# Kernel optimization log

Measured on AMD Instinct MI355X. Metric: run time of the kernel, lower is better.

Reference implementation:

```python
import jax, jax.numpy as jnp
import numpy as np

N = 100000
E = 1600000
IN_DIM = 128
OUT_DIM = 64


def setup_inputs() -> dict:
    key = jax.random.key(0)
    k_h, k_ei, k_ew, k_W, k_a = jax.random.split(key, 5)
    h = jax.random.normal(k_h, (N, IN_DIM), dtype=jnp.float32)
    edge_index = jax.random.randint(k_ei, (2, E), 0, N, dtype=jnp.int64)
    edge_weight = jax.random.uniform(k_ew, (E,), dtype=jnp.float32)
    # nn.Linear weights (Kaiming-uniform-ish scale)
    W = jax.random.uniform(k_W, (OUT_DIM, IN_DIM), dtype=jnp.float32,
                           minval=-1.0, maxval=1.0) / np.sqrt(IN_DIM)
    a = jax.random.uniform(k_a, (2 * OUT_DIM,), dtype=jnp.float32,
                           minval=-1.0, maxval=1.0) / np.sqrt(2 * OUT_DIM)
    return {"h": h, "edge_index": edge_index, "edge_weight": edge_weight,
            "W": W, "a": a}


def reference(h, edge_index, edge_weight, W, a):
    # Faithful translation of _GATConvSparse.forward (inference; dropout = identity).
    n = h.shape[0]
    src, dst = edge_index[0], edge_index[1]
    Wh = h @ W.T                                  # (N, out_dim)
    d = Wh.shape[1]
    # a(cat([Wh[src], Wh[dst]])) == Wh[src] @ a[:d] + Wh[dst] @ a[d:]
    alpha = Wh[src] @ a[:d] + Wh[dst] @ a[d:]     # (E,)
    alpha = alpha * edge_weight
    # Buggy-but-faithful 'softmax': segment-sum raw scores onto dst nodes...
    alpha_node = jax.ops.segment_sum(alpha, dst, num_segments=n)   # (N,)
    alpha_exp = jnp.exp(alpha_node - alpha_node.max())             # (N,)
    # ...then normalize per-edge exp(src) by sum of exp(src) over each dst segment.
    denom = jax.ops.segment_sum(alpha_exp[src], dst, num_segments=n)  # (N,)
    alpha_norm = alpha_exp[src] / (denom[dst] + 1e-9)              # (E,)
    out = jax.ops.segment_sum(alpha_norm[:, None] * Wh[src], dst,
                              num_segments=n)                      # (N, out_dim)
    return jax.nn.elu(out)
```

## Files before the change

kernel.cpp:

```cpp
#include <hip/hip_runtime.h>
#include <math.h>

#define Nn 100000
#define Ee 1600000
#define IND 128
#define OUTD 64
#define DPB 64
#define NB 1563
#define CAP 1536
#define GB 1563
#define EB_BLOCKS 391
#define AFIX 1048576.0f

using bf16x8 = __attribute__((ext_vector_type(8))) short;
using f32x4 = __attribute__((ext_vector_type(4))) float;

__device__ __forceinline__ unsigned short f2bf(float f) {
    unsigned u = __float_as_uint(f);
    u = u + 0x7FFFu + ((u >> 16) & 1u);
    return (unsigned short)(u >> 16);
}
__device__ __forceinline__ float bf2f(unsigned short h) {
    return __uint_as_float(((unsigned)h) << 16);
}

__device__ __forceinline__ bool probe64(const void* __restrict__ ei) {
    const long long* p = (const long long*)ei;
    bool ok = true;
#pragma unroll
    for (int i = 0; i < 8; ++i) {
        long long v = p[i];
        ok = ok && (v >= 0 && v < Nn);
    }
    return ok;
}

__device__ __forceinline__ void load_edge(const void* ei, int e, bool is64,
                                          int& s, int& d) {
    if (is64) {
        const long long* p = (const long long*)ei;
        s = (int)p[e];
        d = (int)p[Ee + e];
    } else {
        const int* p = (const int*)ei;
        s = p[e];
        d = p[Ee + e];
    }
}

__device__ __forceinline__ int load_dst(const void* ei, int e, bool is64) {
    if (is64) return (int)((const long long*)ei)[Ee + e];
    return ((const int*)ei)[Ee + e];
}

__global__ __launch_bounds__(256) void k_fused(
    const float* __restrict__ h, const float* __restrict__ W,
    const float* __restrict__ a, unsigned short* __restrict__ Whb,
    float* __restrict__ s1, float* __restrict__ s2,
    const void* __restrict__ ei, int* __restrict__ bcount) {
    __shared__ unsigned short Ash[64][136];
    __shared__ unsigned short Wsh[64][136];
    __shared__ float al[2 * OUTD];
    int bid = blockIdx.x;
    int t = threadIdx.x;

    if (bid < GB) {
        int R = bid * 64;
        for (int i = t; i < 2048; i += 256) {
            float4 v = ((const float4*)W)[i];
            int r = i >> 5, c = (i & 31) << 2;
            unsigned lo = (unsigned)f2bf(v.x) | ((unsigned)f2bf(v.y) << 16);
            unsigned hi = (unsigned)f2bf(v.z) | ((unsigned)f2bf(v.w) << 16);
            *(uint2*)&Wsh[r][c] = make_uint2(lo, hi);
        }
        if (t < 32) ((float4*)al)[t] = ((const float4*)a)[t];
        for (int i = t; i < 2048; i += 256) {
            int r = i >> 5, c = (i & 31) << 2;
            int n = R + r;
            float4 v = make_float4(0.f, 0.f, 0.f, 0.f);
            if (n < Nn) v = ((const float4*)(h + (size_t)n * IND))[i & 31];
            unsigned lo = (unsigned)f2bf(v.x) | ((unsigned)f2bf(v.y) << 16);
            unsigned hi = (unsigned)f2bf(v.z) | ((unsigned)f2bf(v.w) << 16);
            *(uint2*)&Ash[r][c] = make_uint2(lo, hi);
        }
        __syncthreads();

        int w = t >> 6, l = t & 63;
        int li = l & 15, lg = l >> 4;
        f32x4 acc[4];
#pragma unroll
        for (int nt = 0; nt < 4; ++nt) acc[nt] = (f32x4){0.f, 0.f, 0.f, 0.f};
#pragma unroll
        for (int kk = 0; kk < 4; ++kk) {
            bf16x8 af = *(const bf16x8*)&Ash[w * 16 + li][kk * 32 + lg * 8];
#pragma unroll
            for (int nt = 0; nt < 4; ++nt) {
                bf16x8 bf = *(const bf16x8*)&Wsh[nt * 16 + li][kk * 32 + lg * 8];
                acc[nt] = __builtin_amdgcn_mfma_f32_16x16x32_bf16(af, bf,
                                                                  acc[nt],
                                                                  0, 0, 0);
            }
        }
        float p1[4] = {0.f, 0.f, 0.f, 0.f};
        float p2[4] = {0.f, 0.f, 0.f, 0.f};
#pragma unroll
        for (int nt = 0; nt < 4; ++nt) {
            float a1v = al[nt * 16 + li];
            float a2v = al[OUTD + nt * 16 + li];
#pragma unroll
            for (int r = 0; r < 4; ++r) {
                float v = acc[nt][r];
                p1[r] += v * a1v;
                p2[r] += v * a2v;
                int row = R + w * 16 + lg * 4 + r;
                if (row < Nn)
                    Whb[(size_t)row * OUTD + nt * 16 + li] = f2bf(v);
            }
        }
#pragma unroll
        for (int r = 0; r < 4; ++r) {
#pragma unroll
            for (int m = 1; m < 16; m <<= 1) {
                p1[r] += __shfl_xor(p1[r], m, 64);
                p2[r] += __shfl_xor(p2[r], m, 64);
            }
        }
        if (li < 4) {
            int row = R + w * 16 + lg * 4 + li;
            if (row < Nn) {
                s1[row] = p1[li];
                s2[row] = p2[li];
            }
        }
    } else {
        int* cnt = (int*)&Ash[0][0];
        for (int i = t; i < NB; i += 256) cnt[i] = 0;
        __syncthreads();
        bool is64 = probe64(ei);
        int base = (bid - GB) * 4096;
#pragma unroll
        for (int i = 0; i < 16; ++i) {
            int e = base + i * 256 + t;
            if (e < Ee) atomicAdd(&cnt[load_dst(ei, e, is64) >> 6], 1);
        }
        __syncthreads();
        for (int i = t; i < NB; i += 256) {
            int c = cnt[i];
            if (c) atomicAdd(bcount + i, c);
        }
    }
}

__global__ __launch_bounds__(1024) void k_scan(
    const int* __restrict__ bcount, int* __restrict__ boff,
    int* __restrict__ bcursor) {
    __shared__ int sd[1024];
    int t = threadIdx.x;
    int i0 = 2 * t, i1 = 2 * t + 1;
    int v0 = (i0 < NB) ? bcount[i0] : 0;
    int v1 = (i1 < NB) ? bcount[i1] : 0;
    int pair = v0 + v1;
    sd[t] = pair;
    __syncthreads();
    for (int off = 1; off < 1024; off <<= 1) {
        int add = (t >= off) ? sd[t - off] : 0;
        __syncthreads();
        sd[t] += add;
        __syncthreads();
    }
    int excl = sd[t] - pair;
    if (i0 < NB) {
        boff[i0] = excl;
        bcursor[i0] = excl;
    }
    if (i1 < NB) {
        boff[i1] = excl + v0;
        bcursor[i1] = excl + v0;
    }
    if (t == 0) boff[NB] = Ee;
}

__global__ __launch_bounds__(512) void k_binscatter(
    const void* __restrict__ ei, const float* __restrict__ ew,
    const float* __restrict__ s1, const float* __restrict__ s2,
    int* __restrict__ bcursor, uint2* __restrict__ bins) {
    __shared__ int cnt[NB];
    __shared__ int gbase[NB];
    for (int i = threadIdx.x; i < NB; i += 512) cnt[i] = 0;
    __syncthreads();
    bool is64 = probe64(ei);
    int base = blockIdx.x * 4096;
    unsigned rx[8];
    int ryi[8];
    int rb[8];
    int rk[8];
#pragma unroll
    for (int i = 0; i < 8; ++i) {
        int e = base + i * 512 + threadIdx.x;
        rb[i] = -1;
        rx[i] = 0;
        ryi[i] = 0;
        rk[i] = 0;
        if (e < Ee) {
            int s, d;
            load_edge(ei, e, is64, s, d);
            float alpha = (s1[s] + s2[d]) * ew[e];
            ryi[i] = (int)rintf(alpha * AFIX);
            int b = d >> 6;
            rb[i] = b;
            rk[i] = atomicAdd(&cnt[b], 1);
            rx[i] = (unsigned)s | ((unsigned)(d & 63) << 17);
        }
    }
    __syncthreads();
    for (int i = threadIdx.x; i < NB; i += 512) {
        int c = cnt[i];
        if (c) gbase[i] = atomicAdd(bcursor + i, c);
    }
    __syncthreads();
#pragma unroll
    for (int i = 0; i < 8; ++i) {
        if (rb[i] >= 0) {
            bins[gbase[rb[i]] + rk[i]] = make_uint2(rx[i], (unsigned)ryi[i]);
        }
    }
}

__global__ __launch_bounds__(256) void k_balpha(
    const uint2* __restrict__ bins, const int* __restrict__ boff,
    float* __restrict__ ae) {
    __shared__ int anl[DPB];
    int b = blockIdx.x;
    int t = threadIdx.x;
    if (t < DPB) anl[t] = 0;
    __syncthreads();
    int e0 = boff[b], e1 = boff[b + 1];
    for (int k = e0 + t; k < e1; k += 256) {
        uint2 r = bins[k];
        atomicAdd(&anl[r.x >> 17], (int)r.y);
    }
    __syncthreads();
    if (t < DPB) {
        int n = b * DPB + t;
        if (n < Nn) ae[n] = expf((float)anl[t] * (1.f / AFIX));
    }
}

__global__ __launch_bounds__(256, 6) void k_agg(
    const uint2* __restrict__ bins, const int* __restrict__ boff,
    const float* __restrict__ ae, const unsigned short* __restrict__ Whb,
    float* __restrict__ out) {
    __shared__ uint2 lrec[CAP];
    __shared__ int cnt[DPB];
    __shared__ int sbase[DPB];
    int b = blockIdx.x;
    int t = threadIdx.x;
    int lane = t & 63;
    int wave = t >> 6;
    int half = lane >> 5;
    int hl = lane & 31;
    int e0 = boff[b], e1 = boff[b + 1];
    int total = e1 - e0;
    const unsigned* whb32 = (const unsigned*)Whb;

    if (t < DPB) cnt[t] = 0;
    __syncthreads();

    if (total <= CAP) {
        unsigned su[CAP / 256];
        float sa[CAP / 256];
        int srk[CAP / 256];
#pragma unroll
        for (int i = 0; i < CAP / 256; ++i) {
            int k = e0 + i * 256 + t;
            srk[i] = -1;
            su[i] = 0;
            sa[i] = 0.f;
            if (k < e1) {
                uint2 r = bins[k];
                srk[i] = atomicAdd(&cnt[r.x >> 17], 1);
                su[i] = r.x;
                sa[i] = ae[r.x & 0x1FFFF];
            }
        }
        __syncthreads();
        if (t < DPB) {
            int v = cnt[t];
#pragma unroll
            for (int d = 1; d < DPB; d <<= 1) {
                int u = __shfl_up(v, d, 64);
                if ((t & 63) >= d) v += u;
            }
            sbase[t] = v;
        }
        __syncthreads();
#pragma unroll
        for (int i = 0; i < CAP / 256; ++i) {
            if (srk[i] >= 0) {
                int dloc = su[i] >> 17;
                int pos = sbase[dloc] - cnt[dloc] + srk[i];
                lrec[pos] = make_uint2(su[i], __float_as_uint(sa[i]));
            }
        }
        __syncthreads();

        for (int d = wave * 16; d < wave * 16 + 16; ++d) {
            int k1 = sbase[d];
            int k = k1 - cnt[d];
            float2 acc = make_float2(0.f, 0.f);
            float den = 0.f;
            for (; k + 7 < k1; k += 8) {
                uint2 rA = lrec[k + half];
                uint2 rB = lrec[k + 2 + half];
                uint2 rC = lrec[k + 4 + half];
                uint2 rD = lrec[k + 6 + half];
                unsigned wA = whb32[(rA.x & 0x1FFFF) * 32 + hl];
                unsigned wB = whb32[(rB.x & 0x1FFFF) * 32 + hl];
                unsigned wC = whb32[(rC.x & 0x1FFFF) * 32 + hl];
                unsigned wD = whb32[(rD.x & 0x1FFFF) * 32 + hl];
                float aA = __uint_as_float(rA.y);
                float aB = __uint_as_float(rB.y);
                float aC = __uint_as_float(rC.y);
                float aD = __uint_as_float(rD.y);
                acc.x += aA * __uint_as_float(wA << 16);
                acc.y += aA * __uint_as_float(wA & 0xFFFF0000u);
                acc.x += aB * __uint_as_float(wB << 16);
                acc.y += aB * __uint_as_float(wB & 0xFFFF0000u);
                acc.x += aC * __uint_as_float(wC << 16);
                acc.y += aC * __uint_as_float(wC & 0xFFFF0000u);
                acc.x += aD * __uint_as_float(wD << 16);
                acc.y += aD * __uint_as_float(wD & 0xFFFF0000u);
                den += (aA + aB) + (aC + aD);
            }
            for (; k + 1 < k1; k += 2) {
                uint2 rA = lrec[k + half];
                unsigned wA = whb32[(rA.x & 0x1FFFF) * 32 + hl];
                float aA = __uint_as_float(rA.y);
                acc.x += aA * __uint_as_float(wA << 16);
                acc.y += aA * __uint_as_float(wA & 0xFFFF0000u);
                den += aA;
            }
            if (k < k1) {
                uint2 rA = lrec[k];
                unsigned wA = whb32[(rA.x & 0x1FFFF) * 32 + hl];
                float aA = half ? 0.f : __uint_as_float(rA.y);
                acc.x += aA * __uint_as_float(wA << 16);
                acc.y += aA * __uint_as_float(wA & 0xFFFF0000u);
                den += aA;
            }
            float ax = acc.x + __shfl_xor(acc.x, 32, 64);
            float ay = acc.y + __shfl_xor(acc.y, 32, 64);
            float dn = den + __shfl_xor(den, 32, 64);
            if (half == 0) {
                int n = b * DPB + d;
                if (n < Nn) {
                    float inv = 1.f / (dn + 1e-9f);
                    float vx = ax * inv;
                    float vy = ay * inv;
                    vx = vx > 0.f ? vx : expm1f(vx);
                    vy = vy > 0.f ? vy : expm1f(vy);
                    *(float2*)&out[(size_t)n * OUTD + hl * 2] =
                        make_float2(vx, vy);
                }
            }
        }
    } else {
        for (int j = 0; j < 16; ++j) {
            int dloc = wave * 16 + j;
            int n = b * DPB + dloc;
            if (n >= Nn) continue;
            float aa = 0.f, dd = 0.f;
            for (int k = e0; k < e1; ++k) {
                uint2 r = bins[k];
                if ((int)(r.x >> 17) == dloc) {
                    int s = r.x & 0x1FFFF;
                    float a = ae[s];
                    aa += a * bf2f(Whb[(size_t)s * OUTD + lane]);
                    dd += a;
                }
            }
            float v = aa / (dd + 1e-9f);
            v = v > 0.f ? v : expm1f(v);
            out[(size_t)n * OUTD + lane] = v;
        }
    }
}

extern "C" void kernel_launch(void* const* d_in, const int* in_sizes, int n_in,
                              void* d_out, int out_size, void* d_ws,
                              size_t ws_size, hipStream_t stream) {
    const float* h = (const float*)d_in[0];
    const void* ei = d_in[1];
    const float* ew = (const float*)d_in[2];
    const float* W = (const float*)d_in[3];
    const float* a = (const float*)d_in[4];
    float* out = (float*)d_out;

    unsigned short* Whb = (unsigned short*)d_ws;
    float* s1 = (float*)(Whb + (size_t)Nn * OUTD);
    float* s2 = s1 + Nn;
    float* ae = s2 + Nn;
    int* bcount = (int*)(ae + Nn);
    int* boff = bcount + 2048;
    int* bcursor = boff + 2048;
    uint2* bins = (uint2*)(bcursor + 2048);

    hipMemsetAsync(bcount, 0, 2048 * sizeof(int), stream);

    k_fused<<<GB + EB_BLOCKS, 256, 0, stream>>>(h, W, a, Whb, s1, s2, ei,
                                                bcount);
    k_scan<<<1, 1024, 0, stream>>>(bcount, boff, bcursor);
    k_binscatter<<<EB_BLOCKS, 512, 0, stream>>>(ei, ew, s1, s2, bcursor, bins);
    k_balpha<<<NB, 256, 0, stream>>>(bins, boff, ae);
    k_agg<<<NB, 256, 0, stream>>>(bins, boff, ae, Whb, out);
}
```

Measured before the change: 121.0 us.

## Split aggregation blocks into half-bins and deepen gather unrolling

The aggregation kernel now launches two blocks per 64-node bin. Each block keeps only the edges whose destination falls in its 32-node half, which halves the shared-memory staging buffer and allows 8 blocks per CU. The inner gather loop now issues up to 8 independent Wh loads per iteration to raise memory-level parallelism. The cost is that each block still scans every edge in the bin, so bin records are read twice, and there is a fallback path when a half exceeds the local capacity.

```diff
diff --git a/kernel.cpp b/kernel.cpp
--- a/kernel.cpp
+++ b/kernel.cpp
@@ -7,7 +7,8 @@
 #define OUTD 64
 #define DPB 64
 #define NB 1563
-#define CAP 1536
+#define SCANCAP 1536
+#define LCAP 1024
 #define GB 1563
 #define EB_BLOCKS 391
 #define AFIX 1048576.0f
@@ -246,14 +247,32 @@
     }
 }
 
-__global__ __launch_bounds__(256, 6) void k_agg(
+#define AGG_BODY(NR)                                                         \
+    {                                                                        \
+        uint2 rr[NR];                                                        \
+        unsigned ww[NR];                                                     \
+        _Pragma("unroll") for (int j = 0; j < NR; ++j)                       \
+            rr[j] = lrec[k + 2 * j + half];                                  \
+        _Pragma("unroll") for (int j = 0; j < NR; ++j)                       \
+            ww[j] = whb32[(rr[j].x & 0x1FFFF) * 32 + hl];                    \
+        _Pragma("unroll") for (int j = 0; j < NR; ++j) {                     \
+            float aa = __uint_as_float(rr[j].y);                             \
+            acc.x += aa * __uint_as_float(ww[j] << 16);                      \
+            acc.y += aa * __uint_as_float(ww[j] & 0xFFFF0000u);              \
+            den += aa;                                                       \
+        }                                                                    \
+    }
+
+__global__ __launch_bounds__(256, 8) void k_agg(
     const uint2* __restrict__ bins, const int* __restrict__ boff,
     const float* __restrict__ ae, const unsigned short* __restrict__ Whb,
     float* __restrict__ out) {
-    __shared__ uint2 lrec[CAP];
-    __shared__ int cnt[DPB];
-    __shared__ int sbase[DPB];
-    int b = blockIdx.x;
+    __shared__ uint2 lrec[LCAP];
+    __shared__ int cnt[32];
+    __shared__ int sbase[32];
+    int bid = blockIdx.x;
+    int b = bid >> 1;
+    int H = (bid & 1) << 5;
     int t = threadIdx.x;
     int lane = t & 63;
     int wave = t >> 6;
@@ -263,83 +282,61 @@
     int total = e1 - e0;
     const unsigned* whb32 = (const unsigned*)Whb;
 
-    if (t < DPB) cnt[t] = 0;
-    __syncthreads();
-
-    if (total <= CAP) {
-        unsigned su[CAP / 256];
-        float sa[CAP / 256];
-        int srk[CAP / 256];
-#pragma unroll
-        for (int i = 0; i < CAP / 256; ++i) {
+    if (t < 32) cnt[t] = 0;
+    __syncthreads();
+
+    bool ok = (total <= SCANCAP);
+    unsigned su[SCANCAP / 256];
+    float sa[SCANCAP / 256];
+    int srk[SCANCAP / 256];
+    if (ok) {
+#pragma unroll
+        for (int i = 0; i < SCANCAP / 256; ++i) {
             int k = e0 + i * 256 + t;
             srk[i] = -1;
-            su[i] = 0;
-            sa[i] = 0.f;
             if (k < e1) {
                 uint2 r = bins[k];
-                srk[i] = atomicAdd(&cnt[r.x >> 17], 1);
-                su[i] = r.x;
-                sa[i] = ae[r.x & 0x1FFFF];
-            }
-        }
-        __syncthreads();
-        if (t < DPB) {
+                int lloc = (int)(r.x >> 17) - H;
+                if ((unsigned)lloc < 32u) {
+                    srk[i] = atomicAdd(&cnt[lloc], 1);
+                    su[i] = r.x;
+                    sa[i] = ae[r.x & 0x1FFFF];
+                }
+            }
+        }
+        __syncthreads();
+        if (t < 32) {
             int v = cnt[t];
 #pragma unroll
-            for (int d = 1; d < DPB; d <<= 1) {
+            for (int d = 1; d < 32; d <<= 1) {
                 int u = __shfl_up(v, d, 64);
-                if ((t & 63) >= d) v += u;
+                if (t >= d) v += u;
             }
             sbase[t] = v;
         }
         __syncthreads();
-#pragma unroll
-        for (int i = 0; i < CAP / 256; ++i) {
+        ok = (sbase[31] <= LCAP);
+    }
+
+    if (ok) {
+#pragma unroll
+        for (int i = 0; i < SCANCAP / 256; ++i) {
             if (srk[i] >= 0) {
-                int dloc = su[i] >> 17;
-                int pos = sbase[dloc] - cnt[dloc] + srk[i];
+                int lloc = (int)(su[i] >> 17) - H;
+                int pos = sbase[lloc] - cnt[lloc] + srk[i];
                 lrec[pos] = make_uint2(su[i], __float_as_uint(sa[i]));
             }
         }
         __syncthreads();
 
-        for (int d = wave * 16; d < wave * 16 + 16; ++d) {
+        for (int d = wave * 8; d < wave * 8 + 8; ++d) {
             int k1 = sbase[d];
             int k = k1 - cnt[d];
             float2 acc = make_float2(0.f, 0.f);
             float den = 0.f;
-            for (; k + 7 < k1; k += 8) {
-                uint2 rA = lrec[k + half];
-                uint2 rB = lrec[k + 2 + half];
-                uint2 rC = lrec[k + 4 + half];
-                uint2 rD = lrec[k + 6 + half];
-                unsigned wA = whb32[(rA.x & 0x1FFFF) * 32 + hl];
-                unsigned wB = whb32[(rB.x & 0x1FFFF) * 32 + hl];
-                unsigned wC = whb32[(rC.x & 0x1FFFF) * 32 + hl];
-                unsigned wD = whb32[(rD.x & 0x1FFFF) * 32 + hl];
-                float aA = __uint_as_float(rA.y);
-                float aB = __uint_as_float(rB.y);
-                float aC = __uint_as_float(rC.y);
-                float aD = __uint_as_float(rD.y);
-                acc.x += aA * __uint_as_float(wA << 16);
-                acc.y += aA * __uint_as_float(wA & 0xFFFF0000u);
-                acc.x += aB * __uint_as_float(wB << 16);
-                acc.y += aB * __uint_as_float(wB & 0xFFFF0000u);
-                acc.x += aC * __uint_as_float(wC << 16);
-                acc.y += aC * __uint_as_float(wC & 0xFFFF0000u);
-                acc.x += aD * __uint_as_float(wD << 16);
-                acc.y += aD * __uint_as_float(wD & 0xFFFF0000u);
-                den += (aA + aB) + (aC + aD);
-            }
-            for (; k + 1 < k1; k += 2) {
-                uint2 rA = lrec[k + half];
-                unsigned wA = whb32[(rA.x & 0x1FFFF) * 32 + hl];
-                float aA = __uint_as_float(rA.y);
-                acc.x += aA * __uint_as_float(wA << 16);
-                acc.y += aA * __uint_as_float(wA & 0xFFFF0000u);
-                den += aA;
-            }
+            for (; k + 15 < k1; k += 16) AGG_BODY(8);
+            for (; k + 7 < k1; k += 8) AGG_BODY(4);
+            for (; k + 1 < k1; k += 2) AGG_BODY(1);
             if (k < k1) {
                 uint2 rA = lrec[k];
                 unsigned wA = whb32[(rA.x & 0x1FFFF) * 32 + hl];
@@ -352,7 +349,7 @@
             float ay = acc.y + __shfl_xor(acc.y, 32, 64);
             float dn = den + __shfl_xor(den, 32, 64);
             if (half == 0) {
-                int n = b * DPB + d;
+                int n = b * DPB + H + d;
                 if (n < Nn) {
                     float inv = 1.f / (dn + 1e-9f);
                     float vx = ax * inv;
@@ -365,8 +362,8 @@
             }
         }
     } else {
-        for (int j = 0; j < 16; ++j) {
-            int dloc = wave * 16 + j;
+        for (int j = 0; j < 8; ++j) {
+            int dloc = H + wave * 8 + j;
             int n = b * DPB + dloc;
             if (n >= Nn) continue;
             float aa = 0.f, dd = 0.f;
@@ -412,5 +409,5 @@
     k_scan<<<1, 1024, 0, stream>>>(bcount, boff, bcursor);
     k_binscatter<<<EB_BLOCKS, 512, 0, stream>>>(ei, ew, s1, s2, bcursor, bins);
     k_balpha<<<NB, 256, 0, stream>>>(bins, boff, ae);
-    k_agg<<<NB, 256, 0, stream>>>(bins, boff, ae, Whb, out);
-}
+    k_agg<<<2 * NB, 256, 0, stream>>>(bins, boff, ae, Whb, out);
+}
```

Result: no change. 118.7 us (-1.9%).
